# Kernel optimization log

Hardware: AMD Instinct MI355X
Metric: run time of the kernel (lower is better)

The kernel has to match this reference:

```python
import jax, jax.numpy as jnp
import numpy as np

N_NODES = 20000
N_EDGES = 320000
D = 128  # d_edge = d_node = d_global


def setup_inputs() -> dict:
    key = jax.random.key(0)
    ks = jax.random.split(key, 8)
    inv = lambda fan_in: 1.0 / np.sqrt(fan_in)
    return {
        "edge_attr": jax.random.normal(ks[0], (N_EDGES, D), dtype=jnp.float32),
        "node_attr": jax.random.normal(ks[1], (N_NODES, D), dtype=jnp.float32),
        "u": jax.random.normal(ks[2], (D,), dtype=jnp.float32),
        "senders": jax.random.randint(ks[3], (N_EDGES,), 0, N_NODES, dtype=jnp.int32),
        "receivers": jax.random.randint(ks[4], (N_EDGES,), 0, N_NODES, dtype=jnp.int32),
        "We": jax.random.normal(ks[5], (4 * D, D), dtype=jnp.float32) * inv(4 * D),
        "be": jnp.zeros((D,), dtype=jnp.float32),
        "Wv": jax.random.normal(ks[6], (3 * D, D), dtype=jnp.float32) * inv(3 * D),
        "bv": jnp.zeros((D,), dtype=jnp.float32),
        "Wu": jax.random.normal(ks[7], (3 * D, D), dtype=jnp.float32) * inv(3 * D),
        "bu": jnp.zeros((D,), dtype=jnp.float32),
    }


def reference(edge_attr, node_attr, u, senders, receivers, We, be, Wv, bv, Wu, bu):
    E = edge_attr.shape[0]
    N = node_attr.shape[0]
    u_e = jnp.broadcast_to(u, (E, u.shape[0]))
    u_v = jnp.broadcast_to(u, (N, u.shape[0]))

    # Edge block: phi_e(e, v_r, v_s, u) -- gather endpoint features per edge
    e_in = jnp.concatenate(
        [edge_attr, node_attr[receivers], node_attr[senders], u_e], axis=-1
    )  # [E, 4D]
    e_new = jax.nn.relu(e_in @ We + be)  # [E, D]

    # rho_ev: sum incoming edges per receiver node (scatter-add)
    aggr_e = jax.ops.segment_sum(e_new, receivers, num_segments=N)  # [N, D]

    # Node block: phi_v(aggr_e, v, u)
    v_in = jnp.concatenate([aggr_e, node_attr, u_v], axis=-1)  # [N, 3D]
    v_new = jax.nn.relu(v_in @ Wv + bv)  # [N, D]

    # Global block: rho_eu / rho_vu = mean, phi_u(aggr_e, aggr_v, u)
    aggr_e_u = jnp.mean(e_new, axis=0)
    aggr_v_u = jnp.mean(v_new, axis=0)
    u_in = jnp.concatenate([aggr_e_u, aggr_v_u, u], axis=-1)  # [3D]
    u_new = jax.nn.relu(u_in @ Wu + bu)  # [D]

    return e_new, v_new, u_new
```

## Files before the change

kernel.cpp:

```cpp
#include <hip/hip_runtime.h>
#include <hip/hip_bf16.h>


#define NN 20000
#define NE 320000
#define DD 128
#define SAS 136
#define SBS 136
#define NBLK 512
#define NTILE 5000

typedef unsigned short u16;
typedef __attribute__((ext_vector_type(8))) short bf16x8;
typedef __attribute__((ext_vector_type(4))) float f32x4;

__device__ __forceinline__ float b2f(unsigned short h) {
  return __uint_as_float(((unsigned int)h) << 16);
}
__device__ __forceinline__ unsigned short f2b(float f) {
  unsigned int u = __float_as_uint(f);
  unsigned int r = (u + 0x7fffu + ((u >> 16) & 1u)) >> 16;
  return (unsigned short)r;
}

__device__ __forceinline__ void mfma_core(const u16* sA, const u16* sBT,
                                          int lane, int w, f32x4 acc[4][2]) {
  int r15 = lane & 15;
  int koff = (lane >> 4) * 8;
#pragma unroll
  for (int k0 = 0; k0 < DD; k0 += 32) {
    bf16x8 a[4], b[2];
#pragma unroll
    for (int mt = 0; mt < 4; ++mt)
      a[mt] = *(const bf16x8*)&sA[(mt * 16 + r15) * SAS + k0 + koff];
#pragma unroll
    for (int nt = 0; nt < 2; ++nt)
      b[nt] = *(const bf16x8*)&sBT[(w * 32 + nt * 16 + r15) * SBS + k0 + koff];
#pragma unroll
    for (int mt = 0; mt < 4; ++mt)
#pragma unroll
      for (int nt = 0; nt < 2; ++nt)
        acc[mt][nt] = __builtin_amdgcn_mfma_f32_16x16x32_bf16(
            a[mt], b[nt], acc[mt][nt], 0, 0, 0);
  }
}

__device__ __forceinline__ void stage_w(u16* sBT, const u16* wsrc, int tid) {
  const uint4* ws = (const uint4*)wsrc;
  for (int i = tid; i < DD * DD / 8; i += 256) {
    int n = i >> 4, kk = (i & 15) * 8;
    *(uint4*)&sBT[n * SBS + kk] = ws[i];
  }
}

__global__ __launch_bounds__(256) void k_setup(const int* recv, int* counts,
                                               const float* We, const float* Wv,
                                               const float* u, const float* be,
                                               const float* bv, u16* wt,
                                               float* ce, float* cv) {
  __shared__ float su[DD];
  int b = blockIdx.x, tid = threadIdx.x;
  if (b < 1250) {
    atomicAdd(&counts[recv[b * 256 + tid]], 1);
  } else if (b < 1255) {
    int m = b - 1250;
    const float* W = (m == 0)   ? We
                     : (m == 1) ? We + 128 * DD
                     : (m == 2) ? We + 256 * DD
                     : (m == 3) ? Wv + 128 * DD
                                : Wv;
    u16* o = wt + (size_t)m * DD * DD;
    for (int i = tid; i < DD * DD; i += 256) {
      int k = i >> 7, n = i & 127;
      o[n * DD + k] = f2b(W[i]);
    }
  } else {
    if (tid < DD) su[tid] = u[tid];
    __syncthreads();
    if (tid < DD) {
      float a = be[tid], c = bv[tid];
      for (int k = 0; k < DD; ++k) {
        a = fmaf(su[k], We[(384 + k) * DD + tid], a);
        c = fmaf(su[k], Wv[(256 + k) * DD + tid], c);
      }
      ce[tid] = a;
      cv[tid] = c;
    }
  }
}

__global__ void k_scan(const int* counts, int* rowptr, int* cursor) {
  __shared__ int wsum[16];
  __shared__ int carry;
  int tid = threadIdx.x;
  int lane = tid & 63, wv = tid >> 6;
  if (tid == 0) carry = 0;
  __syncthreads();
  for (int base = 0; base < NN; base += 1024) {
    int i = base + tid;
    int v = (i < NN) ? counts[i] : 0;
    int x = v;
    for (int off = 1; off < 64; off <<= 1) {
      int t = __shfl_up(x, off);
      if (lane >= off) x += t;
    }
    if (lane == 63) wsum[wv] = x;
    __syncthreads();
    if (wv == 0 && lane < 16) {
      int y = wsum[lane];
      for (int off = 1; off < 16; off <<= 1) {
        int t = __shfl_up(y, off);
        if (lane >= off) y += t;
      }
      wsum[lane] = y;
    }
    __syncthreads();
    int woff = (wv > 0) ? wsum[wv - 1] : 0;
    int excl = carry + woff + (x - v);
    if (i < NN) {
      rowptr[i] = excl;
      cursor[i] = excl;
    }
    __syncthreads();
    if (tid == 0) carry += wsum[15];
    __syncthreads();
  }
  if (tid == 0) rowptr[NN] = carry;
}

__global__ __launch_bounds__(256) void k_mid(const int* recv, int* cursor,
                                             int* elist, const float* node_attr,
                                             const u16* wt, u16* P) {
  __shared__ __align__(16) u16 sA[64 * SAS];
  __shared__ __align__(16) u16 sBT[DD * SBS];
  int b = blockIdx.x, tid = threadIdx.x;
  if (b < 1250) {
    int e = b * 256 + tid;
    int slot = atomicAdd(&cursor[recv[e]], 1);
    elist[slot] = e;
    return;
  }
  int n0 = (b - 1250) * 64;
  for (int i = tid; i < 64 * DD / 4; i += 256) {
    int rr = i >> 5, cc = (i & 31) * 4;
    float4 a4 = (n0 + rr < NN)
                    ? ((const float4*)node_attr)[(size_t)(n0 + rr) * 32 + (i & 31)]
                    : make_float4(0, 0, 0, 0);
    ushort4 h;
    h.x = f2b(a4.x); h.y = f2b(a4.y); h.z = f2b(a4.z); h.w = f2b(a4.w);
    *(ushort4*)&sA[rr * SAS + cc] = h;
  }
  int lane = tid & 63, w = tid >> 6;
  int c15 = lane & 15, quad = lane >> 4;
  int col0 = w * 32 + c15, col1 = col0 + 16;
  for (int sel = 0; sel < 3; ++sel) {
    __syncthreads();
    stage_w(sBT, wt + (size_t)(1 + sel) * DD * DD, tid);
    __syncthreads();
    f32x4 acc[4][2] = {};
    mfma_core(sA, sBT, lane, w, acc);
#pragma unroll
    for (int mt = 0; mt < 4; ++mt)
#pragma unroll
      for (int r = 0; r < 4; ++r) {
        int n = n0 + mt * 16 + quad * 4 + r;
        if (n < NN) {
          u16* o = &P[(size_t)n * 384 + sel * 128];
          o[col0] = f2b(acc[mt][0][r]);
          o[col1] = f2b(acc[mt][1][r]);
        }
      }
  }
}

__global__ __launch_bounds__(512, 4) void k_edge(const float* edge_attr,
                                                 const u16* wt, const int* elist,
                                                 const int* recv, const int* send,
                                                 const u16* P, const float* ce,
                                                 float* e_out, float* aggr,
                                                 float* sum_e) {
  __shared__ __align__(16) u16 sA[64 * SAS];
  __shared__ __align__(16) u16 sPr[64 * SAS];
  __shared__ __align__(16) u16 sPs[64 * SAS];
  __shared__ int sEid[64], sRecv[64], sSend[64];
  int tid = threadIdx.x;
  int lane = tid & 63, w = tid >> 6;
  int r15 = lane & 15, quad = lane >> 4;
  int koff = quad * 8;
  int col0 = w * 16 + r15;
  int myrow = tid >> 5;
  int mycol = (tid & 31) * 4;

  bf16x8 breg[4];
#pragma unroll
  for (int kk = 0; kk < 4; ++kk)
    breg[kk] =
        *(const bf16x8*)&wt[(size_t)(w * 16 + r15) * DD + kk * 32 + koff];
  float ce0 = ce[col0];

  float4 areg[4];
  int eid4[4];
  int eidN = 0, rcN = 0, sdN = 0;
  int t = blockIdx.x;

  {
    int base = t * 64;
#pragma unroll
    for (int j = 0; j < 4; ++j) eid4[j] = elist[base + myrow + 16 * j];
    if (tid < 64) {
      eidN = elist[base + tid];
      rcN = recv[eidN];
      sdN = send[eidN];
    }
#pragma unroll
    for (int j = 0; j < 4; ++j)
      areg[j] = *(const float4*)&edge_attr[(size_t)eid4[j] * DD + mycol];
  }
  float colsum = 0.f;
  bool first = true;

  for (; t < NTILE; t += NBLK) {
    if (!first) __syncthreads();
    first = false;
#pragma unroll
    for (int j = 0; j < 4; ++j) {
      ushort4 h;
      h.x = f2b(areg[j].x); h.y = f2b(areg[j].y);
      h.z = f2b(areg[j].z); h.w = f2b(areg[j].w);
      *(ushort4*)&sA[(myrow + 16 * j) * SAS + mycol] = h;
    }
    if (tid < 64) {
      sEid[tid] = eidN;
      sRecv[tid] = rcN;
      sSend[tid] = sdN;
    }
    __syncthreads();

    uint4 q[4];
    int pr_[4], pc_[4], ph_[4];
#pragma unroll
    for (int j = 0; j < 4; ++j) {
      int idx = tid + 512 * j;
      int half = idx >> 10;
      int ii = idx & 1023;
      int row = ii >> 4, ch = ii & 15;
      const uint4* src =
          (half == 0) ? (const uint4*)&P[(size_t)sRecv[row] * 384] + ch
                      : (const uint4*)&P[(size_t)sSend[row] * 384 + 128] + ch;
      q[j] = *src;
      pr_[j] = row; pc_[j] = ch; ph_[j] = half;
    }
    int tn = t + NBLK;
    if (tn < NTILE) {
      int base = tn * 64;
#pragma unroll
      for (int j = 0; j < 4; ++j) eid4[j] = elist[base + myrow + 16 * j];
      if (tid < 64) {
        eidN = elist[base + tid];
        rcN = recv[eidN];
        sdN = send[eidN];
      }
#pragma unroll
      for (int j = 0; j < 4; ++j)
        areg[j] = *(const float4*)&edge_attr[(size_t)eid4[j] * DD + mycol];
    }

    f32x4 acc[4] = {};
#pragma unroll
    for (int kk = 0; kk < 4; ++kk) {
      bf16x8 a[4];
#pragma unroll
      for (int mt = 0; mt < 4; ++mt)
        a[mt] = *(const bf16x8*)&sA[(mt * 16 + r15) * SAS + kk * 32 + koff];
#pragma unroll
      for (int mt = 0; mt < 4; ++mt)
        acc[mt] = __builtin_amdgcn_mfma_f32_16x16x32_bf16(a[mt], breg[kk],
                                                          acc[mt], 0, 0, 0);
    }
#pragma unroll
    for (int j = 0; j < 4; ++j) {
      u16* dst = (ph_[j] == 0) ? sPr : sPs;
      *(uint4*)&dst[pr_[j] * SAS + pc_[j] * 8] = q[j];
    }
    __syncthreads();

#pragma unroll
    for (int mt = 0; mt < 4; ++mt)
#pragma unroll
      for (int r = 0; r < 4; ++r) {
        int m = mt * 16 + quad * 4 + r;
        float v = fmaxf(acc[mt][r] + b2f(sPr[m * SAS + col0]) +
                            b2f(sPs[m * SAS + col0]) + ce0,
                        0.f);
        sA[m * SAS + col0] = f2b(v);
      }
    __syncthreads();

    if (tid < 256) {
      int col = tid & 127, half = tid >> 7;
      int r0 = half * 32;
      float run = 0.f;
      int prev = sRecv[r0];
      for (int r = r0; r < r0 + 32; ++r) {
        int cur = sRecv[r];
        float v = b2f(sA[r * SAS + col]);
        if (cur != prev) {
          atomicAdd(&aggr[(size_t)prev * DD + col], run);
          run = 0.f;
          prev = cur;
        }
        run += v;
        colsum += v;
      }
      atomicAdd(&aggr[(size_t)prev * DD + col], run);
    } else {
      int tt = tid - 256;
#pragma unroll
      for (int j = 0; j < 4; ++j) {
        int i = tt + 256 * j;
        int row = i >> 4, ch = (i & 15) * 8;
        uint4 qq = *(const uint4*)&sA[row * SAS + ch];
        float4 f0, f1;
        f0.x = b2f((u16)(qq.x & 0xffff)); f0.y = b2f((u16)(qq.x >> 16));
        f0.z = b2f((u16)(qq.y & 0xffff)); f0.w = b2f((u16)(qq.y >> 16));
        f1.x = b2f((u16)(qq.z & 0xffff)); f1.y = b2f((u16)(qq.z >> 16));
        f1.z = b2f((u16)(qq.w & 0xffff)); f1.w = b2f((u16)(qq.w >> 16));
        float* dst = &e_out[(size_t)sEid[row] * DD + ch];
        *(float4*)dst = f0;
        *(float4*)(dst + 4) = f1;
      }
    }
  }
  if (tid < 256) atomicAdd(&sum_e[tid & 127], colsum);
}

__global__ __launch_bounds__(256) void k_node(const float* aggr, const u16* wt,
                                              const u16* P, const float* cv,
                                              float* v_out, float* sum_v) {
  __shared__ __align__(16) u16 sA[64 * SAS];
  __shared__ __align__(16) u16 sBT[DD * SBS];
  __shared__ float sCol[DD];
  int tid = threadIdx.x;
  int n0 = blockIdx.x * 64;
  stage_w(sBT, wt + (size_t)4 * DD * DD, tid);
  for (int i = tid; i < 64 * DD / 4; i += 256) {
    int rr = i >> 5, cc = (i & 31) * 4;
    float4 a4 = (n0 + rr < NN)
                    ? ((const float4*)aggr)[(size_t)(n0 + rr) * 32 + (i & 31)]
                    : make_float4(0, 0, 0, 0);
    ushort4 h;
    h.x = f2b(a4.x); h.y = f2b(a4.y); h.z = f2b(a4.z); h.w = f2b(a4.w);
    *(ushort4*)&sA[rr * SAS + cc] = h;
  }
  if (tid < DD) sCol[tid] = 0.f;
  __syncthreads();
  int lane = tid & 63, w = tid >> 6;
  f32x4 acc[4][2] = {};
  mfma_core(sA, sBT, lane, w, acc);
  int c15 = lane & 15, quad = lane >> 4;
  int col0 = w * 32 + c15, col1 = col0 + 16;
  float cv0 = cv[col0], cv1 = cv[col1];
  float cs0 = 0.f, cs1 = 0.f;
#pragma unroll
  for (int mt = 0; mt < 4; ++mt)
#pragma unroll
    for (int r = 0; r < 4; ++r) {
      int n = n0 + mt * 16 + quad * 4 + r;
      if (n < NN) {
        const u16* pv = &P[(size_t)n * 384 + 256];
        float v0 = fmaxf(acc[mt][0][r] + b2f(pv[col0]) + cv0, 0.f);
        float v1 = fmaxf(acc[mt][1][r] + b2f(pv[col1]) + cv1, 0.f);
        size_t ob = (size_t)n * DD;
        v_out[ob + col0] = v0;
        v_out[ob + col1] = v1;
        cs0 += v0;
        cs1 += v1;
      }
    }
  atomicAdd(&sCol[col0], cs0);
  atomicAdd(&sCol[col1], cs1);
  __syncthreads();
  if (tid < DD) atomicAdd(&sum_v[tid], sCol[tid]);
}

__global__ void k_global(const float* sumbuf, const float* u, const float* Wu,
                         const float* bu, float* out) {
  __shared__ float sin_[384];
  int j = threadIdx.x;
  sin_[j] = sumbuf[j] * (1.0f / (float)NE);
  sin_[128 + j] = sumbuf[128 + j] * (1.0f / (float)NN);
  sin_[256 + j] = u[j];
  __syncthreads();
  float a = bu[j];
  for (int k = 0; k < 384; ++k) a = fmaf(sin_[k], Wu[k * DD + j], a);
  out[j] = fmaxf(a, 0.f);
}

extern "C" void kernel_launch(void* const* d_in, const int* in_sizes, int n_in,
                              void* d_out, int out_size, void* d_ws,
                              size_t ws_size, hipStream_t stream) {
  const float* edge_attr = (const float*)d_in[0];
  const float* node_attr = (const float*)d_in[1];
  const float* u = (const float*)d_in[2];
  const int* senders = (const int*)d_in[3];
  const int* receivers = (const int*)d_in[4];
  const float* We = (const float*)d_in[5];
  const float* be = (const float*)d_in[6];
  const float* Wv = (const float*)d_in[7];
  const float* bv = (const float*)d_in[8];
  const float* Wu = (const float*)d_in[9];
  const float* bu = (const float*)d_in[10];

  float* e_out = (float*)d_out;
  float* v_out = e_out + (size_t)NE * DD;
  float* u_out = v_out + (size_t)NN * DD;

  int* counts = (int*)d_ws;
  float* sumbuf = (float*)d_ws + NN;
  float* aggr = (float*)d_ws + NN + 256;
  int* rowptr = (int*)d_ws + NN + 256 + NN * DD;
  int* cursor = rowptr + NN + 1;
  int* elist = cursor + NN;
  size_t off = (size_t)(NN + 256 + NN * DD + (NN + 1) + NN + NE);
  off = (off + 3) & ~(size_t)3;
  u16* wt = (u16*)((float*)d_ws + off);
  u16* P = wt + (size_t)5 * DD * DD;
  float* ce = (float*)(P + (size_t)NN * 384);
  float* cv = ce + 128;

  hipMemsetAsync(d_ws, 0, (size_t)(NN + 256 + NN * DD) * 4, stream);
  k_setup<<<1256, 256, 0, stream>>>(receivers, counts, We, Wv, u, be, bv, wt,
                                    ce, cv);
  k_scan<<<1, 1024, 0, stream>>>(counts, rowptr, cursor);
  k_mid<<<1250 + 313, 256, 0, stream>>>(receivers, cursor, elist, node_attr,
                                        wt, P);
  k_edge<<<NBLK, 512, 0, stream>>>(edge_attr, wt, elist, receivers, senders, P,
                                   ce, e_out, aggr, sumbuf);
  k_node<<<(NN + 63) / 64, 256, 0, stream>>>(aggr, wt, P, cv, v_out,
                                             sumbuf + 128);
  k_global<<<1, 128, 0, stream>>>(sumbuf, u, Wu, bu, u_out);
}
```

Measured before the change: 490.2 us.

## Pre-sum gathered receiver/sender projections into one LDS tile and double edge-kernel occupancy

The gathered receiver and sender projections are now added pairwise in registers, rounded to bf16, and written to a single shared tile. This replaces the two separate shared tiles and their two epilogue reads. Freeing that LDS lets the launch bound be raised to 8 blocks per CU and the grid doubled to 1024 blocks. The trade-off is an extra bf16 rounding of the partial sum and fewer tiles per block over which to amortise the prefetch and weight loads.

Result: slower. 627.2 us (+27.9%).

```diff
diff --git a/kernel.cpp b/kernel.cpp
--- a/kernel.cpp
+++ b/kernel.cpp
@@ -7,7 +7,7 @@
 #define DD 128
 #define SAS 136
 #define SBS 136
-#define NBLK 512
+#define NBLK 1024
 #define NTILE 5000
 
 typedef unsigned short u16;
@@ -21,6 +21,11 @@
   unsigned int u = __float_as_uint(f);
   unsigned int r = (u + 0x7fffu + ((u >> 16) & 1u)) >> 16;
   return (unsigned short)r;
+}
+__device__ __forceinline__ unsigned int addpk(unsigned int a, unsigned int b) {
+  float lo = __uint_as_float(a << 16) + __uint_as_float(b << 16);
+  float hi = __uint_as_float(a & 0xffff0000u) + __uint_as_float(b & 0xffff0000u);
+  return (unsigned int)f2b(lo) | (((unsigned int)f2b(hi)) << 16);
 }
 
 __device__ __forceinline__ void mfma_core(const u16* sA, const u16* sBT,
@@ -173,15 +178,14 @@
   }
 }
 
-__global__ __launch_bounds__(512, 4) void k_edge(const float* edge_attr,
+__global__ __launch_bounds__(512, 8) void k_edge(const float* edge_attr,
                                                  const u16* wt, const int* elist,
                                                  const int* recv, const int* send,
                                                  const u16* P, const float* ce,
                                                  float* e_out, float* aggr,
                                                  float* sum_e) {
   __shared__ __align__(16) u16 sA[64 * SAS];
-  __shared__ __align__(16) u16 sPr[64 * SAS];
-  __shared__ __align__(16) u16 sPs[64 * SAS];
+  __shared__ __align__(16) u16 sPQ[64 * SAS];
   __shared__ int sEid[64], sRecv[64], sSend[64];
   int tid = threadIdx.x;
   int lane = tid & 63, w = tid >> 6;
@@ -190,6 +194,8 @@
   int col0 = w * 16 + r15;
   int myrow = tid >> 5;
   int mycol = (tid & 31) * 4;
+  int grow = tid >> 4;
+  int gch = tid & 15;
 
   bf16x8 breg[4];
 #pragma unroll
@@ -236,19 +242,12 @@
     }
     __syncthreads();
 
-    uint4 q[4];
-    int pr_[4], pc_[4], ph_[4];
-#pragma unroll
-    for (int j = 0; j < 4; ++j) {
-      int idx = tid + 512 * j;
-      int half = idx >> 10;
-      int ii = idx & 1023;
-      int row = ii >> 4, ch = ii & 15;
-      const uint4* src =
-          (half == 0) ? (const uint4*)&P[(size_t)sRecv[row] * 384] + ch
-                      : (const uint4*)&P[(size_t)sSend[row] * 384 + 128] + ch;
-      q[j] = *src;
-      pr_[j] = row; pc_[j] = ch; ph_[j] = half;
+    uint4 q1[2], q2[2];
+#pragma unroll
+    for (int j = 0; j < 2; ++j) {
+      int row = grow + 32 * j;
+      q1[j] = *((const uint4*)&P[(size_t)sRecv[row] * 384] + gch);
+      q2[j] = *((const uint4*)&P[(size_t)sSend[row] * 384 + 128] + gch);
     }
     int tn = t + NBLK;
     if (tn < NTILE) {
@@ -278,9 +277,14 @@
                                                           acc[mt], 0, 0, 0);
     }
 #pragma unroll
-    for (int j = 0; j < 4; ++j) {
-      u16* dst = (ph_[j] == 0) ? sPr : sPs;
-      *(uint4*)&dst[pr_[j] * SAS + pc_[j] * 8] = q[j];
+    for (int j = 0; j < 2; ++j) {
+      int row = grow + 32 * j;
+      uint4 o;
+      o.x = addpk(q1[j].x, q2[j].x);
+      o.y = addpk(q1[j].y, q2[j].y);
+      o.z = addpk(q1[j].z, q2[j].z);
+      o.w = addpk(q1[j].w, q2[j].w);
+      *(uint4*)&sPQ[row * SAS + gch * 8] = o;
     }
     __syncthreads();
 
@@ -289,9 +293,7 @@
 #pragma unroll
       for (int r = 0; r < 4; ++r) {
         int m = mt * 16 + quad * 4 + r;
-        float v = fmaxf(acc[mt][r] + b2f(sPr[m * SAS + col0]) +
-                            b2f(sPs[m * SAS + col0]) + ce0,
-                        0.f);
+        float v = fmaxf(acc[mt][r] + b2f(sPQ[m * SAS + col0]) + ce0, 0.f);
         sA[m * SAS + col0] = f2b(v);
       }
     __syncthreads();
```
